# Optimization experiments

Hardware: AMD Instinct MI355X
Metric: run time of the kernel (lower is better)

Reference implementation:

```python
import jax, jax.numpy as jnp
import numpy as np

ALPHA = 0.001  # plasticity learning rate from the source module
B, I, H = 64, 512, 1024
D = I + H


def _xavier(k, shape):
    fan_out, fan_in = shape
    lim = float(np.sqrt(6.0 / (fan_in + fan_out)))
    return jax.random.uniform(k, shape, minval=-lim, maxval=lim, dtype=jnp.float32)


def setup_inputs() -> dict:
    key = jax.random.key(0)
    ks = jax.random.split(key, 9)
    inputs = jax.random.normal(ks[0], (B, I), dtype=jnp.float32)
    hidden = 0.1 * jax.random.normal(ks[1], (B, H), dtype=jnp.float32)
    # per-sample plastic fast weights (nonzero to exercise the matvec path)
    wih = 0.01 * jax.random.normal(ks[2], (B, H, D), dtype=jnp.float32)
    Wih_a = _xavier(ks[3], (H, D))
    Wih_b = _xavier(ks[4], (H, D))
    Wih_c = _xavier(ks[5], (H, D))
    Wih_d = _xavier(ks[6], (H, D))
    bih = jnp.zeros((H,), dtype=jnp.float32)
    W_dop = _xavier(ks[7], (H, D))
    b_dop = jnp.zeros((H,), dtype=jnp.float32)
    return {"inputs": inputs, "hidden": hidden, "wih": wih,
            "Wih_a": Wih_a, "Wih_b": Wih_b, "Wih_c": Wih_c, "Wih_d": Wih_d,
            "bih": bih, "W_dop": W_dop, "b_dop": b_dop}


def reference(inputs, hidden, wih, Wih_a, Wih_b, Wih_c, Wih_d, bih, W_dop, b_dop):
    # x = cat(inputs, hidden): [B, D]
    x = jnp.concatenate([inputs, hidden], axis=1)
    # dopamine_signal is computed in the source but never used downstream;
    # kept here for fidelity (XLA will DCE it).
    _dopamine = jax.nn.sigmoid(x @ W_dop.T + b_dop)  # noqa: F841
    # batched matvec over the plastic fast weights: [B,H]
    new_hidden = jnp.tanh(jnp.einsum('bj,bkj->bk', x, wih) + bih)
    y = new_hidden[:, :, None]   # [B, H, 1]
    xb = x[:, None, :]           # [B, 1, D]
    # Hebbian outer-product update (the two 'ones' bmms are just broadcasts)
    wih_new = wih + ALPHA * (y * xb * Wih_a + xb * Wih_b + y * Wih_c + Wih_d)
    return new_hidden, wih_new
```

## Files before the change

kernel.cpp:

```cpp
#include <hip/hip_runtime.h>

constexpr int Bn = 64;
constexpr int In = 512;
constexpr int Hn = 1024;
constexpr int Dn = 1536;
constexpr float ALPHA = 0.001f;
constexpr int RPW = 8;

typedef float nfloat4 __attribute__((ext_vector_type(4)));

__global__ __launch_bounds__(256) void prnn_fused_kernel(
    const float* __restrict__ inputs,
    const float* __restrict__ hidden,
    const float* __restrict__ wih,
    const float* __restrict__ Wa,
    const float* __restrict__ Wb,
    const float* __restrict__ Wc,
    const float* __restrict__ Wd,
    const float* __restrict__ bih,
    float* __restrict__ out_hidden,
    float* __restrict__ out_wih)
{
    __shared__ float4 sW[4 * (Dn / 4)];

    const int k     = blockIdx.x >> 1;
    const int bbase = (blockIdx.x & 1) * 32;
    const int tid   = threadIdx.x;

    {
        const float4* wa4 = (const float4*)(Wa + (size_t)k * Dn);
        const float4* wb4 = (const float4*)(Wb + (size_t)k * Dn);
        const float4* wc4 = (const float4*)(Wc + (size_t)k * Dn);
        const float4* wd4 = (const float4*)(Wd + (size_t)k * Dn);
        #pragma unroll
        for (int e = 0; e < 2; ++e) {
            const int i = tid + e * 256;
            if (i < 384) {
                sW[i]        = wa4[i];
                sW[384 + i]  = wb4[i];
                sW[768 + i]  = wc4[i];
                sW[1152 + i] = wd4[i];
            }
        }
    }
    __syncthreads();

    const int wave = tid >> 6;
    const int lane = tid & 63;
    const int b0   = bbase + wave * RPW;
    const float bk = bih[k];
    const int base = lane * 4;

    float4 wbuf[3][6];
    float4 xbuf[2][6];

    auto load_w = [&](int r, float4 (&w)[6]) {
        const float* __restrict__ wrow = wih + ((size_t)(b0 + r) * Hn + k) * Dn;
        #pragma unroll
        for (int c = 0; c < 6; ++c)
            w[c] = *(const float4*)(wrow + c * 256 + base);
    };
    auto load_x = [&](int r, float4 (&x)[6]) {
        const int b = b0 + r;
        const float* __restrict__ xin  = inputs + b * In;
        const float* __restrict__ xhid = hidden + b * Hn;
        #pragma unroll
        for (int c = 0; c < 6; ++c) {
            const int idx = c * 256 + base;
            x[c] = (c < 2) ? *(const float4*)(xin + idx)
                           : *(const float4*)(xhid + (idx - In));
        }
    };

    load_w(0, wbuf[0]);
    load_w(1, wbuf[1]);
    load_x(0, xbuf[0]);

    #pragma unroll
    for (int r = 0; r < RPW; ++r) {
        if (r + 1 < RPW) load_x(r + 1, xbuf[(r + 1) & 1]);
        if (r + 2 < RPW) load_w(r + 2, wbuf[(r + 2) % 3]);

        float4 (&w)[6] = wbuf[r % 3];
        float4 (&x)[6] = xbuf[r & 1];

        float acc = 0.0f;
        #pragma unroll
        for (int c = 0; c < 6; ++c)
            acc += w[c].x * x[c].x + w[c].y * x[c].y
                 + w[c].z * x[c].z + w[c].w * x[c].w;

        #pragma unroll
        for (int off = 32; off > 0; off >>= 1)
            acc += __shfl_xor(acc, off, 64);

        const float y = tanhf(acc + bk);
        const int b = b0 + r;
        if (lane == 0) out_hidden[b * Hn + k] = y;

        float* __restrict__ orow = out_wih + ((size_t)b * Hn + k) * Dn;
        #pragma unroll
        for (int c = 0; c < 6; ++c) {
            const int e = c * 64 + lane;
            const float4 a4 = sW[e];
            const float4 b4 = sW[384 + e];
            const float4 c4 = sW[768 + e];
            const float4 d4 = sW[1152 + e];
            nfloat4 o;
            o.x = w[c].x + ALPHA * (y * x[c].x * a4.x + x[c].x * b4.x + y * c4.x + d4.x);
            o.y = w[c].y + ALPHA * (y * x[c].y * a4.y + x[c].y * b4.y + y * c4.y + d4.y);
            o.z = w[c].z + ALPHA * (y * x[c].z * a4.z + x[c].z * b4.z + y * c4.z + d4.z);
            o.w = w[c].w + ALPHA * (y * x[c].w * a4.w + x[c].w * b4.w + y * c4.w + d4.w);
            __builtin_nontemporal_store(o, (nfloat4*)(orow + c * 256 + base));
        }
    }
}

extern "C" void kernel_launch(void* const* d_in, const int* in_sizes, int n_in,
                              void* d_out, int out_size, void* d_ws, size_t ws_size,
                              hipStream_t stream) {
    const float* inputs = (const float*)d_in[0];
    const float* hidden = (const float*)d_in[1];
    const float* wih    = (const float*)d_in[2];
    const float* Wa     = (const float*)d_in[3];
    const float* Wb     = (const float*)d_in[4];
    const float* Wc     = (const float*)d_in[5];
    const float* Wd     = (const float*)d_in[6];
    const float* bih    = (const float*)d_in[7];

    float* out_hidden = (float*)d_out;
    float* out_wih    = (float*)d_out + (size_t)Bn * Hn;

    prnn_fused_kernel<<<dim3(Hn * 2), dim3(256), 0, stream>>>(
        inputs, hidden, wih, Wa, Wb, Wc, Wd, bih, out_hidden, out_wih);
}
```

Baseline: 161.0 us.

## Stage wih rows and x through LDS via async global_load_lds double buffering

Replaces the register-based triple/double buffering of wih rows and x with direct global-to-LDS DMA (global_load_lds) into two per-wave LDS slots. Hand-placed vmcnt waits and sched barriers pace the pipeline. The goal is to cut VGPR pressure and overlap loads with compute. The cost is a much larger LDS allocation (about 120 KB per block), which limits the CU to one block and cuts wave occupancy for a bandwidth-bound kernel. The hard-coded vmcnt values also depend on the exact count of outstanding loads and stores.

```diff
diff --git a/kernel.cpp b/kernel.cpp
--- a/kernel.cpp
+++ b/kernel.cpp
@@ -6,8 +6,15 @@
 constexpr int Dn = 1536;
 constexpr float ALPHA = 0.001f;
 constexpr int RPW = 8;
+constexpr int LDS_FLOATS = 6144 + 4 * 2 * 3072;
 
 typedef float nfloat4 __attribute__((ext_vector_type(4)));
+
+__device__ __forceinline__ void dma16(const float* g, float* l) {
+    __builtin_amdgcn_global_load_lds(
+        (const __attribute__((address_space(1))) void*)g,
+        (__attribute__((address_space(3))) void*)l, 16, 0, 0);
+}
 
 __global__ __launch_bounds__(256) void prnn_fused_kernel(
     const float* __restrict__ inputs,
@@ -21,13 +28,16 @@
     float* __restrict__ out_hidden,
     float* __restrict__ out_wih)
 {
-    __shared__ float4 sW[4 * (Dn / 4)];
+    extern __shared__ float lds[];
 
     const int k     = blockIdx.x >> 1;
     const int bbase = (blockIdx.x & 1) * 32;
     const int tid   = threadIdx.x;
+    const int wv    = tid >> 6;
+    const int lane  = tid & 63;
 
     {
+        float4* s4 = (float4*)lds;
         const float4* wa4 = (const float4*)(Wa + (size_t)k * Dn);
         const float4* wb4 = (const float4*)(Wb + (size_t)k * Dn);
         const float4* wc4 = (const float4*)(Wc + (size_t)k * Dn);
@@ -36,53 +46,52 @@
         for (int e = 0; e < 2; ++e) {
             const int i = tid + e * 256;
             if (i < 384) {
-                sW[i]        = wa4[i];
-                sW[384 + i]  = wb4[i];
-                sW[768 + i]  = wc4[i];
-                sW[1152 + i] = wd4[i];
+                s4[i]        = wa4[i];
+                s4[384 + i]  = wb4[i];
+                s4[768 + i]  = wc4[i];
+                s4[1152 + i] = wd4[i];
             }
         }
     }
     __syncthreads();
 
-    const int wave = tid >> 6;
-    const int lane = tid & 63;
-    const int b0   = bbase + wave * RPW;
+    const int b0   = bbase + wv * RPW;
     const float bk = bih[k];
-    const int base = lane * 4;
+    float* const slot0 = &lds[6144 + (wv * 2 + 0) * 3072];
+    float* const slot1 = &lds[6144 + (wv * 2 + 1) * 3072];
 
-    float4 wbuf[3][6];
-    float4 xbuf[2][6];
-
-    auto load_w = [&](int r, float4 (&w)[6]) {
-        const float* __restrict__ wrow = wih + ((size_t)(b0 + r) * Hn + k) * Dn;
+    auto dma_row = [&](int r, float* slot) {
+        const int b = b0 + r;
+        const float* __restrict__ wrow = wih + ((size_t)b * Hn + k) * Dn;
         #pragma unroll
-        for (int c = 0; c < 6; ++c)
-            w[c] = *(const float4*)(wrow + c * 256 + base);
-    };
-    auto load_x = [&](int r, float4 (&x)[6]) {
-        const int b = b0 + r;
-        const float* __restrict__ xin  = inputs + b * In;
-        const float* __restrict__ xhid = hidden + b * Hn;
+        for (int c = 0; c < 6; ++c) dma16(wrow + c * 256 + lane * 4, slot + c * 256);
+        const float* __restrict__ xin = inputs + b * In;
         #pragma unroll
-        for (int c = 0; c < 6; ++c) {
-            const int idx = c * 256 + base;
-            x[c] = (c < 2) ? *(const float4*)(xin + idx)
-                           : *(const float4*)(xhid + (idx - In));
-        }
+        for (int c = 0; c < 2; ++c) dma16(xin + c * 256 + lane * 4, slot + 1536 + c * 256);
+        const float* __restrict__ xh = hidden + b * Hn;
+        #pragma unroll
+        for (int c = 0; c < 4; ++c) dma16(xh + c * 256 + lane * 4, slot + 2048 + c * 256);
     };
 
-    load_w(0, wbuf[0]);
-    load_w(1, wbuf[1]);
-    load_x(0, xbuf[0]);
+    dma_row(0, slot0);
+    dma_row(1, slot1);
 
     #pragma unroll
     for (int r = 0; r < RPW; ++r) {
-        if (r + 1 < RPW) load_x(r + 1, xbuf[(r + 1) & 1]);
-        if (r + 2 < RPW) load_w(r + 2, wbuf[(r + 2) % 3]);
+        __builtin_amdgcn_sched_barrier(0);
+        if (r == 0)            asm volatile("s_waitcnt vmcnt(12)" ::: "memory");
+        else if (r == RPW - 1) asm volatile("s_waitcnt vmcnt(7)"  ::: "memory");
+        else                   asm volatile("s_waitcnt vmcnt(19)" ::: "memory");
+        __builtin_amdgcn_sched_barrier(0);
 
-        float4 (&w)[6] = wbuf[r % 3];
-        float4 (&x)[6] = xbuf[r & 1];
+        const float* slot = (r & 1) ? slot1 : slot0;
+        float4 w[6], x[6];
+        #pragma unroll
+        for (int c = 0; c < 6; ++c)
+            w[c] = *(const float4*)(slot + c * 256 + lane * 4);
+        #pragma unroll
+        for (int c = 0; c < 6; ++c)
+            x[c] = *(const float4*)(slot + 1536 + c * 256 + lane * 4);
 
         float acc = 0.0f;
         #pragma unroll
@@ -102,17 +111,22 @@
         #pragma unroll
         for (int c = 0; c < 6; ++c) {
             const int e = c * 64 + lane;
-            const float4 a4 = sW[e];
-            const float4 b4 = sW[384 + e];
-            const float4 c4 = sW[768 + e];
-            const float4 d4 = sW[1152 + e];
+            const float4 a4 = ((const float4*)lds)[e];
+            const float4 b4 = ((const float4*)lds)[384 + e];
+            const float4 c4 = ((const float4*)lds)[768 + e];
+            const float4 d4 = ((const float4*)lds)[1152 + e];
             nfloat4 o;
             o.x = w[c].x + ALPHA * (y * x[c].x * a4.x + x[c].x * b4.x + y * c4.x + d4.x);
             o.y = w[c].y + ALPHA * (y * x[c].y * a4.y + x[c].y * b4.y + y * c4.y + d4.y);
             o.z = w[c].z + ALPHA * (y * x[c].z * a4.z + x[c].z * b4.z + y * c4.z + d4.z);
             o.w = w[c].w + ALPHA * (y * x[c].w * a4.w + x[c].w * b4.w + y * c4.w + d4.w);
-            __builtin_nontemporal_store(o, (nfloat4*)(orow + c * 256 + base));
+            __builtin_nontemporal_store(o, (nfloat4*)(orow + c * 256 + lane * 4));
         }
+
+        asm volatile("" ::: "memory");
+        __builtin_amdgcn_sched_barrier(0);
+        if (r + 2 < RPW) dma_row(r + 2, (r & 1) ? slot1 : slot0);
+        asm volatile("" ::: "memory");
     }
 }
 
@@ -131,6 +145,11 @@
     float* out_hidden = (float*)d_out;
     float* out_wih    = (float*)d_out + (size_t)Bn * Hn;
 
-    prnn_fused_kernel<<<dim3(Hn * 2), dim3(256), 0, stream>>>(
+    const size_t lds_bytes = (size_t)LDS_FLOATS * sizeof(float);
+    (void)hipFuncSetAttribute((const void*)prnn_fused_kernel,
+                              hipFuncAttributeMaxDynamicSharedMemorySize,
+                              (int)lds_bytes);
+
+    prnn_fused_kernel<<<dim3(Hn * 2), dim3(256), lds_bytes, stream>>>(
         inputs, hidden, wih, Wa, Wb, Wc, Wd, bih, out_hidden, out_wih);
 }
```

New measurement: 200.8 us. +24.7%, slower.
